# Kernel tuning notes

Measured on AMD Instinct MI355X. Metric: run time of the kernel, lower is better.

## Reference

```python
import jax, jax.numpy as jnp
import numpy as np
from math import log

MODEL_DIM = 512
NUM_HEADS = 8
DIM_HEAD = 64
INNER = NUM_HEADS * DIM_HEAD
B, L = 8, 1024
EPS = 1e-5


def setup_inputs() -> dict:
    key = jax.random.key(0)
    ks = jax.random.split(key, 9)
    x = jax.random.normal(ks[0], (B, L, MODEL_DIM), dtype=jnp.float32)
    gamma = jnp.ones((MODEL_DIM,), jnp.float32)
    beta = jnp.zeros((MODEL_DIM,), jnp.float32)
    w_qkv = jax.random.normal(ks[1], (3 * INNER, MODEL_DIM), jnp.float32) * (MODEL_DIM ** -0.5)
    b_qkv = jnp.zeros((3 * INNER,), jnp.float32)
    w_pos = jax.random.normal(ks[2], (INNER, MODEL_DIM), jnp.float32) * (MODEL_DIM ** -0.5)
    w_out = jax.random.normal(ks[3], (MODEL_DIM, INNER), jnp.float32) * (INNER ** -0.5)
    b_out = jnp.zeros((MODEL_DIM,), jnp.float32)
    # xavier_uniform for (num_heads, dim_head)
    bound = (6.0 / (NUM_HEADS + DIM_HEAD)) ** 0.5
    u_bias = jax.random.uniform(ks[4], (NUM_HEADS, DIM_HEAD), jnp.float32, -bound, bound)
    v_bias = jax.random.uniform(ks[5], (NUM_HEADS, DIM_HEAD), jnp.float32, -bound, bound)
    return {"x": x, "gamma": gamma, "beta": beta, "w_qkv": w_qkv, "b_qkv": b_qkv,
            "w_pos": w_pos, "w_out": w_out, "b_out": b_out, "u_bias": u_bias, "v_bias": v_bias}


def _rel_pos_emb(seq_len, d):
    # (L, D): (i - j) scaled by sinusoid frequencies, then cos on even cols, sin on odd cols
    rel = (jnp.arange(seq_len, dtype=jnp.float32)[:, None]
           - jnp.arange(d, dtype=jnp.float32)[None, :])
    freqs = jnp.exp(-jnp.arange(0, 2 * d, 2, dtype=jnp.float32) * (log(10000.0) / MODEL_DIM))
    angle = rel * freqs[None, :]
    even = (jnp.arange(d) % 2) == 0
    return jnp.where(even[None, :], jnp.cos(angle), jnp.sin(angle))  # (L, D)


def reference(x, gamma, beta, w_qkv, b_qkv, w_pos, w_out, b_out, u_bias, v_bias):
    b, l, d = x.shape
    h, dh = NUM_HEADS, DIM_HEAD
    # LayerNorm
    mu = jnp.mean(x, axis=-1, keepdims=True)
    var = jnp.mean(jnp.square(x - mu), axis=-1, keepdims=True)
    xn = (x - mu) * jax.lax.rsqrt(var + EPS) * gamma + beta
    # relative position embedding, identical per batch element
    pe = _rel_pos_emb(l, d)                      # (L, D)
    pos = (pe @ w_pos.T).reshape(l, h, dh)       # (L, H, Dh)
    pos = jnp.transpose(pos, (1, 0, 2))          # (H, L, Dh)
    # qkv
    qkv = xn @ w_qkv.T + b_qkv                   # (B, L, 3*inner)
    q, k, v = jnp.split(qkv, 3, axis=-1)
    def to_heads(t):
        return jnp.transpose(t.reshape(b, l, h, dh), (0, 2, 1, 3))  # (B,H,L,Dh)
    q, k, v = to_heads(q), to_heads(k), to_heads(v)
    scale = dh ** -0.5
    content = jnp.einsum('bhld,bhmd->bhlm', q + u_bias[None, :, None, :], k)
    pos_score = jnp.einsum('bhld,hmd->bhlm', q + v_bias[None, :, None, :], pos)
    attn = jax.nn.softmax((content + pos_score) * scale, axis=-1)
    out = jnp.einsum('bhlm,bhmd->bhld', attn, v)
    out = jnp.transpose(out, (0, 2, 1, 3)).reshape(b, l, h * dh)
    return out @ w_out.T + b_out  # dropout p=0.0 -> identity
```

## Files before the change

### kernel.cpp

```cpp
#include <hip/hip_runtime.h>
#include <math.h>

static constexpr int Bn = 8, Ln = 1024, Dm = 512, Hn = 8, DhN = 64;

typedef short bf16x8 __attribute__((ext_vector_type(8)));
typedef float f32x4 __attribute__((ext_vector_type(4)));
typedef _Float16 f16x4 __attribute__((ext_vector_type(4)));
typedef _Float16 f16x8 __attribute__((ext_vector_type(8)));
typedef unsigned int u32x4 __attribute__((ext_vector_type(4)));
typedef unsigned short u16x8 __attribute__((ext_vector_type(8)));

#define QSCALE 0.1803368801111137f

static __device__ __forceinline__ unsigned short f2b(float f) {
  union { float f; unsigned int u; } x;
  x.f = f;
  unsigned int u = x.u;
  unsigned int r = (u + 0x7FFFu + ((u >> 16) & 1u)) >> 16;
  return (unsigned short)r;
}
static __device__ __forceinline__ float b2f(unsigned short u) {
  union { unsigned int u; float f; } x;
  x.u = ((unsigned int)u) << 16;
  return x.f;
}

#define GLDS16(g, l)                                                        \
  __builtin_amdgcn_global_load_lds((const __attribute__((address_space(1))) void*)(g), \
                                   (__attribute__((address_space(3))) void*)(l), 16, 0, 0)

__global__ __launch_bounds__(256) void prep1(const float* __restrict__ x,
                                             const float* __restrict__ gamma,
                                             const float* __restrict__ beta,
                                             unsigned short* __restrict__ xn,
                                             unsigned short* __restrict__ pe,
                                             const float* __restrict__ wq, unsigned short* __restrict__ wqb,
                                             const float* __restrict__ wp, unsigned short* __restrict__ wpb,
                                             const float* __restrict__ wo, unsigned short* __restrict__ wob) {
  int b = blockIdx.x;
  int t = threadIdx.x;
  if (b < 8192) {
    const float2 v = *(const float2*)(x + (size_t)b * Dm + t * 2);
    float s = v.x + v.y;
    float sq = v.x * v.x + v.y * v.y;
#pragma unroll
    for (int off = 32; off > 0; off >>= 1) {
      s += __shfl_down(s, off);
      sq += __shfl_down(sq, off);
    }
    __shared__ float red[8];
    int wave = t >> 6, lane = t & 63;
    if (lane == 0) { red[wave * 2] = s; red[wave * 2 + 1] = sq; }
    __syncthreads();
    float S = red[0] + red[2] + red[4] + red[6];
    float SQ = red[1] + red[3] + red[5] + red[7];
    float mu = S * (1.0f / Dm);
    float var = SQ * (1.0f / Dm) - mu * mu;
    float rstd = rsqrtf(var + 1e-5f);
    int c = t * 2;
    ushort2 o;
    o.x = f2b((v.x - mu) * rstd * gamma[c] + beta[c]);
    o.y = f2b((v.y - mu) * rstd * gamma[c + 1] + beta[c + 1]);
    *(ushort2*)(xn + (size_t)b * Dm + c) = o;
  } else if (b < 10240) {
    int idx = (b - 8192) * 256 + t;
    int l = idx >> 9, k = idx & 511;
    float freq = __expf(-0.0359778921f * (float)k);
    float angle = (float)(l - k) * freq;
    pe[idx] = f2b((k & 1) ? __sinf(angle) : __cosf(angle));
  } else {
    int cb = b - 10240;
    const float* src;
    unsigned short* dst;
    int off;
    if (cb < 768) { src = wq; dst = wqb; off = cb; }
    else if (cb < 1024) { src = wp; dst = wpb; off = cb - 768; }
    else { src = wo; dst = wob; off = cb - 1024; }
    int i = off * 256 + t;
    float4 v = *(const float4*)(src + (size_t)i * 4);
    ushort4 o;
    o.x = f2b(v.x); o.y = f2b(v.y); o.z = f2b(v.z); o.w = f2b(v.w);
    *(ushort4*)(dst + (size_t)i * 4) = o;
  }
}

__global__ __launch_bounds__(256, 6) void gemm2(const unsigned short* __restrict__ Ain,
                                                const unsigned short* __restrict__ Bwin,
                                                const float* __restrict__ biasin,
                                                unsigned short* __restrict__ oq,
                                                unsigned short* __restrict__ ok,
                                                unsigned short* __restrict__ ov,
                                                const unsigned short* __restrict__ A2,
                                                const unsigned short* __restrict__ B2,
                                                unsigned short* __restrict__ outp) {
  int by = blockIdx.y, bx = blockIdx.x;
  int mode = 0;
  const unsigned short* A = Ain;
  const unsigned short* Bw = Bwin;
  const float* bias = biasin;
  if (by < 64) {
    int lid = by * 24 + bx;
    int i = lid >> 3;
    by = (lid & 7) * 8 + i / 24;
    bx = i % 24;
  } else {
    if (bx >= 8) return;
    A = A2; Bw = B2; bias = nullptr; mode = 1; by -= 64;
  }
  const int K = 512;
  __shared__ alignas(16) unsigned short As[128 * 64];
  __shared__ alignas(16) unsigned short Bs[64 * 64];
  const int t = threadIdx.x;
  const int lane = t & 63, w = t >> 6;
  const int c = lane & 15, q8 = lane >> 4;
  const int wm = (w & 1) * 64, wn = (w >> 1) * 32;
  const int m0 = by * 128, n0 = bx * 64;

  f32x4 acc[4][2];
#pragma unroll
  for (int i = 0; i < 4; ++i)
#pragma unroll
    for (int j = 0; j < 2; ++j) acc[i][j] = (f32x4){0.f, 0.f, 0.f, 0.f};

  const int srow = lane >> 3;
  const int sgr = (lane & 7) ^ srow;

  for (int k0 = 0; k0 < K; k0 += 64) {
    __syncthreads();
#pragma unroll
    for (int s = 0; s < 4; ++s) {
      int r = s * 32 + w * 8 + srow;
      GLDS16(A + (size_t)(m0 + r) * K + k0 + sgr * 8, As + (s * 256 + w * 64 + lane) * 8);
    }
#pragma unroll
    for (int s = 0; s < 2; ++s) {
      int r = s * 32 + w * 8 + srow;
      GLDS16(Bw + (size_t)(n0 + r) * K + k0 + sgr * 8, Bs + (s * 256 + w * 64 + lane) * 8);
    }
    __syncthreads();
#pragma unroll
    for (int kk = 0; kk < 2; ++kk) {
      bf16x8 a[4], b[2];
      const int q = kk * 4 + q8;
#pragma unroll
      for (int i = 0; i < 4; ++i) {
        int r = wm + i * 16 + c;
        a[i] = *(const bf16x8*)&As[(r * 8 + (q ^ (r & 7))) * 8];
      }
#pragma unroll
      for (int j = 0; j < 2; ++j) {
        int r = wn + j * 16 + c;
        b[j] = *(const bf16x8*)&Bs[(r * 8 + (q ^ (r & 7))) * 8];
      }
#pragma unroll
      for (int i = 0; i < 4; ++i)
#pragma unroll
        for (int j = 0; j < 2; ++j)
          acc[i][j] = __builtin_amdgcn_mfma_f32_16x16x32_bf16(a[i], b[j], acc[i][j], 0, 0, 0);
    }
  }
#pragma unroll
  for (int i = 0; i < 4; ++i) {
#pragma unroll
    for (int r = 0; r < 4; ++r) {
      int m = m0 + wm + i * 16 + q8 * 4 + r;
#pragma unroll
      for (int j = 0; j < 2; ++j) {
        int n = n0 + wn + j * 16 + c;
        float val = acc[i][j][r] + (bias ? bias[n] : 0.0f);
        if (mode == 0) {
          int part = n >> 9, h = (n >> 6) & 7, dh = n & 63;
          int bb = m >> 10, l = m & 1023;
          size_t idx = (size_t)((bb * 8 + h) * 1024 + l) * 64 + dh;
          if (part == 0) {
            oq[idx] = f2b(val * QSCALE);
          } else if (part == 1) {
            ok[idx] = f2b(val);
          } else {
            union { _Float16 h; unsigned short u; } cv;
            cv.h = (_Float16)val;
            ov[idx] = cv.u;
          }
        } else {
          int h = n >> 6, dh = n & 63;
          outp[(size_t)(h * 1024 + m) * 64 + dh] = f2b(val);
        }
      }
    }
  }
}

__global__ __launch_bounds__(256, 8) void gemm_mfma(const unsigned short* __restrict__ Ain,
                                                    const unsigned short* __restrict__ Bwin,
                                                    const float* __restrict__ biasin,
                                                    float* __restrict__ outfin,
                                                    int K) {
  int by = blockIdx.y, bx = blockIdx.x;
  {
    int NBX = gridDim.x;
    int lid = by * NBX + bx;
    int i = lid >> 3;
    by = (lid & 7) * 16 + i / NBX;
    bx = i % NBX;
  }
  const unsigned short* A = Ain;
  const unsigned short* Bw = Bwin;
  const float* bias = biasin;
  float* outf = outfin;
  __shared__ alignas(16) unsigned short As[64 * 64];
  __shared__ alignas(16) unsigned short Bs[64 * 64];
  const int t = threadIdx.x;
  const int lane = t & 63, w = t >> 6;
  const int c = lane & 15, q8 = lane >> 4;
  const int wm = (w & 1) * 32, wn = (w >> 1) * 32;
  const int m0 = by * 64, n0 = bx * 64;

  f32x4 acc[2][2];
#pragma unroll
  for (int i = 0; i < 2; ++i)
#pragma unroll
    for (int j = 0; j < 2; ++j) acc[i][j] = (f32x4){0.f, 0.f, 0.f, 0.f};

  const int srow = lane >> 3;
  const int sgr = (lane & 7) ^ srow;

  for (int k0 = 0; k0 < K; k0 += 64) {
    __syncthreads();
#pragma unroll
    for (int j = 0; j < 2; ++j) {
      int r = j * 32 + w * 8 + srow;
      GLDS16(A + (size_t)(m0 + r) * K + k0 + sgr * 8, As + (j * 256 + w * 64 + lane) * 8);
      GLDS16(Bw + (size_t)(n0 + r) * K + k0 + sgr * 8, Bs + (j * 256 + w * 64 + lane) * 8);
    }
    __syncthreads();
#pragma unroll
    for (int kk = 0; kk < 2; ++kk) {
      bf16x8 a[2], b[2];
      const int q = kk * 4 + q8;
#pragma unroll
      for (int i = 0; i < 2; ++i) {
        int r = wm + i * 16 + c;
        a[i] = *(const bf16x8*)&As[(r * 8 + (q ^ (r & 7))) * 8];
      }
#pragma unroll
      for (int j = 0; j < 2; ++j) {
        int r = wn + j * 16 + c;
        b[j] = *(const bf16x8*)&Bs[(r * 8 + (q ^ (r & 7))) * 8];
      }
#pragma unroll
      for (int i = 0; i < 2; ++i)
#pragma unroll
        for (int j = 0; j < 2; ++j)
          acc[i][j] = __builtin_amdgcn_mfma_f32_16x16x32_bf16(a[i], b[j], acc[i][j], 0, 0, 0);
    }
  }
#pragma unroll
  for (int i = 0; i < 2; ++i) {
#pragma unroll
    for (int r = 0; r < 4; ++r) {
      int m = m0 + wm + i * 16 + q8 * 4 + r;
#pragma unroll
      for (int j = 0; j < 2; ++j) {
        int n = n0 + wn + j * 16 + c;
        outf[(size_t)m * 512 + n] = acc[i][j][r] + bias[n];
      }
    }
  }
}

__global__ __launch_bounds__(256) void prep2(unsigned short* __restrict__ kbuf,
                                             const unsigned short* __restrict__ posbf,
                                             const float* __restrict__ ub,
                                             const float* __restrict__ vbb,
                                             float* __restrict__ biasout,
                                             const unsigned short* __restrict__ v,
                                             unsigned short* __restrict__ vt) {
  int b = blockIdx.x;
  int t = threadIdx.x;
  if (b < 2048) {
    int g = b * 32 + (t >> 3);
    int s = t & 7;
    int h = (g >> 10) & 7;
    int m = g & 1023;
    u16x8 kv8 = *(const u16x8*)(kbuf + (size_t)g * 64 + s * 8);
    u16x8 pv8 = *(const u16x8*)(posbf + (size_t)(h * 1024 + m) * 64 + s * 8);
    f32x4 u0 = *(const f32x4*)(ub + h * 64 + s * 8);
    f32x4 u1 = *(const f32x4*)(ub + h * 64 + s * 8 + 4);
    f32x4 v0 = *(const f32x4*)(vbb + h * 64 + s * 8);
    f32x4 v1 = *(const f32x4*)(vbb + h * 64 + s * 8 + 4);
    float part = 0.0f;
    u16x8 o8;
#pragma unroll
    for (int e = 0; e < 8; ++e) {
      float kf = b2f(kv8[e]);
      float pf = b2f(pv8[e]);
      float ue = (e < 4) ? u0[e] : u1[e - 4];
      float ve = (e < 4) ? v0[e] : v1[e - 4];
      part += ue * kf + ve * pf;
      o8[e] = f2b(kf + pf);
    }
    *(u16x8*)(kbuf + (size_t)g * 64 + s * 8) = o8;
    part += __shfl_xor(part, 1);
    part += __shfl_xor(part, 2);
    part += __shfl_xor(part, 4);
    if (s == 0) biasout[g] = part * QSCALE;
  } else {
    __shared__ unsigned short Ts[64 * 68];
    int bb = b - 2048;
    int bh = bb >> 4, lt = bb & 15;
    const unsigned short* vg = v + (size_t)bh * 65536 + lt * 4096;
#pragma unroll
    for (int s = 0; s < 4; ++s) {
      int idx = t + s * 256;
      int r = idx >> 4, c4 = (idx & 15) << 2;
      *(ushort4*)&Ts[r * 68 + c4] = *(const ushort4*)(vg + r * 64 + c4);
    }
    __syncthreads();
#pragma unroll
    for (int s = 0; s < 4; ++s) {
      int idx = t + s * 256;
      int d = idx >> 4, l4 = (idx & 15) << 2;
      ushort4 o;
      o.x = Ts[(l4 + 0) * 68 + d];
      o.y = Ts[(l4 + 1) * 68 + d];
      o.z = Ts[(l4 + 2) * 68 + d];
      o.w = Ts[(l4 + 3) * 68 + d];
      int pb = ((l4 >> 5) & 1) * 32 + ((l4 >> 2) & 3) * 8 + ((l4 >> 4) & 1) * 4;
      *(ushort4*)(vt + (size_t)bh * 65536 + d * 1024 + lt * 64 + pb) = o;
    }
  }
}

__global__ __launch_bounds__(256, 2) void flash_mfma(const unsigned short* __restrict__ qbf,
                                                     const unsigned short* __restrict__ kbf,
                                                     const unsigned short* __restrict__ vt,
                                                     const float* __restrict__ bias,
                                                     unsigned short* __restrict__ attn_out) {
  __shared__ alignas(16) unsigned short Ks[2][64 * 64];
  __shared__ alignas(16) unsigned short Vs[2][64 * 64];
  __shared__ alignas(16) float Bls[1024];
  const int t = threadIdx.x;
  const int lane = t & 63, w = t >> 6;
  const int c = lane & 15, q8 = lane >> 4;
  const int cc7 = c & 7;
  const int lid = blockIdx.x + (blockIdx.y << 3);
  const int bh = ((lid & 7) << 3) + ((lid >> 3) & 7);
  const int qt = lid >> 6;
  const unsigned short* qg = qbf + (size_t)bh * 65536;
  const unsigned short* kg = kbf + (size_t)bh * 65536;
  const unsigned short* vg = vt + (size_t)bh * 65536;
  const float* bg = bias + (size_t)bh * 1024;

  GLDS16(bg + t * 4, Bls + t * 4);

  bf16x8 bq[2][2];
#pragma unroll
  for (int g = 0; g < 2; ++g) {
    int qlg = qt * 128 + g * 64 + w * 16 + c;
    bq[g][0] = *(const bf16x8*)(qg + (size_t)qlg * 64 + q8 * 8);
    bq[g][1] = *(const bf16x8*)(qg + (size_t)qlg * 64 + 32 + q8 * 8);
  }

  float m_st[2] = {-INFINITY, -INFINITY};
  float l_st[2] = {0.0f, 0.0f};
  f32x4 o[2][4];
#pragma unroll
  for (int g = 0; g < 2; ++g)
#pragma unroll
    for (int i = 0; i < 4; ++i) o[g][i] = (f32x4){0.f, 0.f, 0.f, 0.f};

  const int srow = lane >> 3;
  const int sgr = (lane & 7) ^ srow;
  const int r0 = w * 16 + srow;

  u32x4 pk[2][2], pv[2][2];
#pragma unroll
  for (int h = 0; h < 2; ++h)
#pragma unroll
    for (int j = 0; j < 2; ++j) {
      int r = r0 + j * 8;
      pk[h][j] = *(const u32x4*)(kg + (size_t)(h * 64 + r) * 64 + sgr * 8);
      pv[h][j] = *(const u32x4*)(vg + (size_t)r * 1024 + h * 64 + sgr * 8);
    }

  for (int it = 0; it < 8; ++it) {
    __syncthreads();
#pragma unroll
    for (int h = 0; h < 2; ++h)
#pragma unroll
      for (int j = 0; j < 2; ++j) {
        int r = r0 + j * 8;
        *(u32x4*)&Ks[h][(r * 8 + (lane & 7)) * 8] = pk[h][j];
        *(u32x4*)&Vs[h][(r * 8 + (lane & 7)) * 8] = pv[h][j];
      }
    __syncthreads();
    if (it < 7) {
#pragma unroll
      for (int h = 0; h < 2; ++h)
#pragma unroll
        for (int j = 0; j < 2; ++j) {
          int r = r0 + j * 8;
          pk[h][j] = *(const u32x4*)(kg + (size_t)((it + 1) * 128 + h * 64 + r) * 64 + sgr * 8);
          pv[h][j] = *(const u32x4*)(vg + (size_t)r * 1024 + (it + 1) * 128 + h * 64 + sgr * 8);
        }
    }

    f32x4 sc[2][2][4];
#pragma unroll
    for (int h = 0; h < 2; ++h) {
#pragma unroll
      for (int nt = 0; nt < 4; ++nt) {
        f32x4 ci = *(const f32x4*)&Bls[it * 128 + h * 64 + nt * 16 + q8 * 4];
        const int row = nt * 16 + c;
        bf16x8 ak0 = *(const bf16x8*)&Ks[h][(row * 8 + (q8 ^ cc7)) * 8];
        bf16x8 ak1 = *(const bf16x8*)&Ks[h][(row * 8 + ((q8 + 4) ^ cc7)) * 8];
#pragma unroll
        for (int g = 0; g < 2; ++g) {
          f32x4 z = __builtin_amdgcn_mfma_f32_16x16x32_bf16(ak0, bq[g][0], ci, 0, 0, 0);
          sc[g][h][nt] = __builtin_amdgcn_mfma_f32_16x16x32_bf16(ak1, bq[g][1], z, 0, 0, 0);
        }
      }
    }
    float mx[2];
#pragma unroll
    for (int g = 0; g < 2; ++g) {
      float m = sc[g][0][0][0];
#pragma unroll
      for (int h = 0; h < 2; ++h)
#pragma unroll
        for (int nt = 0; nt < 4; ++nt)
#pragma unroll
          for (int r = 0; r < 4; ++r) m = fmaxf(m, sc[g][h][nt][r]);
      mx[g] = m;
    }
    {
      float s0 = __shfl_xor(mx[0], 16);
      float s1 = __shfl_xor(mx[1], 16);
      mx[0] = fmaxf(mx[0], s0);
      mx[1] = fmaxf(mx[1], s1);
      s0 = __shfl_xor(mx[0], 32);
      s1 = __shfl_xor(mx[1], 32);
      mx[0] = fmaxf(mx[0], s0);
      mx[1] = fmaxf(mx[1], s1);
    }
    f16x8 pf8[2][2][2];
#pragma unroll
    for (int g = 0; g < 2; ++g) {
      float mn = fmaxf(m_st[g], mx[g]);
      float al = __builtin_amdgcn_exp2f(m_st[g] - mn);
      float su = 0.0f;
#pragma unroll
      for (int h = 0; h < 2; ++h)
#pragma unroll
        for (int nt = 0; nt < 4; ++nt)
#pragma unroll
          for (int r = 0; r < 4; ++r) {
            float p = __builtin_amdgcn_exp2f(sc[g][h][nt][r] - mn);
            su += p;
            pf8[g][h][nt >> 1][((nt & 1) << 2) | r] = (_Float16)p;
          }
      l_st[g] = l_st[g] * al + su;
      m_st[g] = mn;
#pragma unroll
      for (int i = 0; i < 4; ++i) o[g][i] *= al;
    }
#pragma unroll
    for (int i = 0; i < 4; ++i) {
      const int row = i * 16 + c;
#pragma unroll
      for (int h = 0; h < 2; ++h) {
        f16x8 va = *(const f16x8*)&Vs[h][(row * 8 + (q8 ^ cc7)) * 8];
        f16x8 vb = *(const f16x8*)&Vs[h][(row * 8 + ((4 + q8) ^ cc7)) * 8];
#pragma unroll
        for (int g = 0; g < 2; ++g) {
          o[g][i] = __builtin_amdgcn_mfma_f32_16x16x32_f16(va, pf8[g][h][0], o[g][i], 0, 0, 0);
          o[g][i] = __builtin_amdgcn_mfma_f32_16x16x32_f16(vb, pf8[g][h][1], o[g][i], 0, 0, 0);
        }
      }
    }
  }
  float lt0 = l_st[0], lt1 = l_st[1];
  {
    float s0 = __shfl_xor(lt0, 16);
    float s1 = __shfl_xor(lt1, 16);
    lt0 += s0; lt1 += s1;
    s0 = __shfl_xor(lt0, 32);
    s1 = __shfl_xor(lt1, 32);
    lt0 += s0; lt1 += s1;
  }
  const int bidx = bh >> 3, h = bh & 7;
#pragma unroll
  for (int g = 0; g < 2; ++g) {
    int qlg = qt * 128 + g * 64 + w * 16 + c;
    float inv = 1.0f / (g == 0 ? lt0 : lt1);
    size_t base = (size_t)(bidx * 1024 + qlg) * 512 + h * 64;
#pragma unroll
    for (int i = 0; i < 4; ++i) {
      ushort4 ov4;
      ov4.x = f2b(o[g][i][0] * inv);
      ov4.y = f2b(o[g][i][1] * inv);
      ov4.z = f2b(o[g][i][2] * inv);
      ov4.w = f2b(o[g][i][3] * inv);
      *(ushort4*)(attn_out + base + i * 16 + q8 * 4) = ov4;
    }
  }
}

extern "C" void kernel_launch(void* const* d_in, const int* in_sizes, int n_in,
                              void* d_out, int out_size, void* d_ws, size_t ws_size,
                              hipStream_t stream) {
  const float* x      = (const float*)d_in[0];
  const float* gamma  = (const float*)d_in[1];
  const float* beta   = (const float*)d_in[2];
  const float* w_qkv  = (const float*)d_in[3];
  const float* b_qkv  = (const float*)d_in[4];
  const float* w_pos  = (const float*)d_in[5];
  const float* w_out  = (const float*)d_in[6];
  const float* b_out  = (const float*)d_in[7];
  const float* u_bias = (const float*)d_in[8];
  const float* v_bias = (const float*)d_in[9];
  float* out = (float*)d_out;

  unsigned short* wsu = (unsigned short*)d_ws;
  unsigned short* xnb   = wsu;
  unsigned short* peb   = wsu + 4194304;
  unsigned short* wqkvb = wsu + 4718592;
  unsigned short* wposb = wsu + 5505024;
  unsigned short* woutb = wsu + 5767168;
  unsigned short* qbf   = wsu + 6291456;
  unsigned short* kbf   = wsu + 10485760;
  unsigned short* vbf   = wsu + 14680064;
  unsigned short* vtb   = wsu + 18874368;
  unsigned short* attnb = wsu + 23068672;
  unsigned short* posbf = wsu + 27262976;
  float* biasb = (float*)(wsu + 28311552);

  prep1<<<11520, 256, 0, stream>>>(x, gamma, beta, xnb, peb,
                                   w_qkv, wqkvb, w_pos, wposb, w_out, woutb);
  gemm2<<<dim3(24, 72), 256, 0, stream>>>(xnb, wqkvb, b_qkv, qbf, kbf, vbf,
                                          peb, wposb, posbf);
  prep2<<<3072, 256, 0, stream>>>(kbf, posbf, u_bias, v_bias, biasb, vbf, vtb);
  flash_mfma<<<dim3(8, 64), 256, 0, stream>>>(qbf, kbf, vtb, biasb, attnb);
  gemm_mfma<<<dim3(8, 128), 256, 0, stream>>>(attnb, woutb, b_out, out, 512);
}
```

Before: 162.1 us.

## Retile QKV GEMM to 64x64 with K=128 steps; vectorize LayerNorm to two rows per block

The QKV/pos GEMM moves from 128x64 tiles with a 64-deep K step to 64x64 tiles with a 128-deep K step. This doubles the grid and halves the per-wave accumulator count, with a 16-way LDS swizzle to match and the occupancy hint lowered to 5. LayerNorm now processes two rows per block using float4 loads and vectorized gamma/beta reads, which halves the block count for that section. The smaller tiles mean less operand reuse per block, traded for more parallelism and fewer K-loop barriers.

```diff
diff --git a/kernel.cpp b/kernel.cpp
--- a/kernel.cpp
+++ b/kernel.cpp
@@ -39,10 +39,12 @@
                                              const float* __restrict__ wo, unsigned short* __restrict__ wob) {
   int b = blockIdx.x;
   int t = threadIdx.x;
-  if (b < 8192) {
-    const float2 v = *(const float2*)(x + (size_t)b * Dm + t * 2);
-    float s = v.x + v.y;
-    float sq = v.x * v.x + v.y * v.y;
+  if (b < 4096) {
+    int row = b * 2 + (t >> 7);
+    int tl = t & 127;
+    const float4 v = *(const float4*)(x + (size_t)row * Dm + tl * 4);
+    float s = v.x + v.y + v.z + v.w;
+    float sq = v.x * v.x + v.y * v.y + v.z * v.z + v.w * v.w;
 #pragma unroll
     for (int off = 32; off > 0; off >>= 1) {
       s += __shfl_down(s, off);
@@ -52,24 +54,29 @@
     int wave = t >> 6, lane = t & 63;
     if (lane == 0) { red[wave * 2] = s; red[wave * 2 + 1] = sq; }
     __syncthreads();
-    float S = red[0] + red[2] + red[4] + red[6];
-    float SQ = red[1] + red[3] + red[5] + red[7];
+    int half = t >> 7;
+    float S = red[half * 4 + 0] + red[half * 4 + 2];
+    float SQ = red[half * 4 + 1] + red[half * 4 + 3];
     float mu = S * (1.0f / Dm);
     float var = SQ * (1.0f / Dm) - mu * mu;
     float rstd = rsqrtf(var + 1e-5f);
-    int c = t * 2;
-    ushort2 o;
-    o.x = f2b((v.x - mu) * rstd * gamma[c] + beta[c]);
-    o.y = f2b((v.y - mu) * rstd * gamma[c + 1] + beta[c + 1]);
-    *(ushort2*)(xn + (size_t)b * Dm + c) = o;
-  } else if (b < 10240) {
-    int idx = (b - 8192) * 256 + t;
+    int c = tl * 4;
+    const float4 g4 = *(const float4*)(gamma + c);
+    const float4 b4 = *(const float4*)(beta + c);
+    ushort4 o;
+    o.x = f2b((v.x - mu) * rstd * g4.x + b4.x);
+    o.y = f2b((v.y - mu) * rstd * g4.y + b4.y);
+    o.z = f2b((v.z - mu) * rstd * g4.z + b4.z);
+    o.w = f2b((v.w - mu) * rstd * g4.w + b4.w);
+    *(ushort4*)(xn + (size_t)row * Dm + c) = o;
+  } else if (b < 6144) {
+    int idx = (b - 4096) * 256 + t;
     int l = idx >> 9, k = idx & 511;
     float freq = __expf(-0.0359778921f * (float)k);
     float angle = (float)(l - k) * freq;
     pe[idx] = f2b((k & 1) ? __sinf(angle) : __cosf(angle));
   } else {
-    int cb = b - 10240;
+    int cb = b - 6144;
     const float* src;
     unsigned short* dst;
     int off;
@@ -84,7 +91,7 @@
   }
 }
 
-__global__ __launch_bounds__(256, 6) void gemm2(const unsigned short* __restrict__ Ain,
+__global__ __launch_bounds__(256, 5) void gemm2(const unsigned short* __restrict__ Ain,
                                                 const unsigned short* __restrict__ Bwin,
                                                 const float* __restrict__ biasin,
                                                 unsigned short* __restrict__ oq,
@@ -98,69 +105,65 @@
   const unsigned short* A = Ain;
   const unsigned short* Bw = Bwin;
   const float* bias = biasin;
-  if (by < 64) {
+  if (by < 128) {
     int lid = by * 24 + bx;
     int i = lid >> 3;
-    by = (lid & 7) * 8 + i / 24;
+    by = (lid & 7) * 16 + i / 24;
     bx = i % 24;
   } else {
     if (bx >= 8) return;
-    A = A2; Bw = B2; bias = nullptr; mode = 1; by -= 64;
+    A = A2; Bw = B2; bias = nullptr; mode = 1; by -= 128;
   }
   const int K = 512;
-  __shared__ alignas(16) unsigned short As[128 * 64];
-  __shared__ alignas(16) unsigned short Bs[64 * 64];
+  __shared__ alignas(16) unsigned short As[64 * 128];
+  __shared__ alignas(16) unsigned short Bs[64 * 128];
   const int t = threadIdx.x;
   const int lane = t & 63, w = t >> 6;
   const int c = lane & 15, q8 = lane >> 4;
-  const int wm = (w & 1) * 64, wn = (w >> 1) * 32;
-  const int m0 = by * 128, n0 = bx * 64;
-
-  f32x4 acc[4][2];
-#pragma unroll
-  for (int i = 0; i < 4; ++i)
+  const int wm = (w & 1) * 32, wn = (w >> 1) * 32;
+  const int m0 = by * 64, n0 = bx * 64;
+
+  f32x4 acc[2][2];
+#pragma unroll
+  for (int i = 0; i < 2; ++i)
 #pragma unroll
     for (int j = 0; j < 2; ++j) acc[i][j] = (f32x4){0.f, 0.f, 0.f, 0.f};
 
-  const int srow = lane >> 3;
-  const int sgr = (lane & 7) ^ srow;
-
-  for (int k0 = 0; k0 < K; k0 += 64) {
-    __syncthreads();
-#pragma unroll
-    for (int s = 0; s < 4; ++s) {
-      int r = s * 32 + w * 8 + srow;
-      GLDS16(A + (size_t)(m0 + r) * K + k0 + sgr * 8, As + (s * 256 + w * 64 + lane) * 8);
-    }
-#pragma unroll
-    for (int s = 0; s < 2; ++s) {
-      int r = s * 32 + w * 8 + srow;
-      GLDS16(Bw + (size_t)(n0 + r) * K + k0 + sgr * 8, Bs + (s * 256 + w * 64 + lane) * 8);
-    }
-    __syncthreads();
-#pragma unroll
-    for (int kk = 0; kk < 2; ++kk) {
-      bf16x8 a[4], b[2];
+  const int srow = t >> 4;
+  const int sgr = (t & 15) ^ srow;
+
+  for (int k0 = 0; k0 < K; k0 += 128) {
+    __syncthreads();
+#pragma unroll
+    for (int p = 0; p < 4; ++p) {
+      int r = p * 16 + srow;
+      GLDS16(A + (size_t)(m0 + r) * K + k0 + sgr * 8, As + (p * 256 + t) * 8);
+      GLDS16(Bw + (size_t)(n0 + r) * K + k0 + sgr * 8, Bs + (p * 256 + t) * 8);
+    }
+    __syncthreads();
+#pragma unroll
+    for (int kk = 0; kk < 4; ++kk) {
+      bf16x8 a[2], b[2];
       const int q = kk * 4 + q8;
 #pragma unroll
-      for (int i = 0; i < 4; ++i) {
+      for (int i = 0; i < 2; ++i) {
         int r = wm + i * 16 + c;
-        a[i] = *(const bf16x8*)&As[(r * 8 + (q ^ (r & 7))) * 8];
+        a[i] = *(const bf16x8*)&As[(r * 16 + (q ^ (r & 15))) * 8];
       }
 #pragma unroll
       for (int j = 0; j < 2; ++j) {
         int r = wn + j * 16 + c;
-        b[j] = *(const bf16x8*)&Bs[(r * 8 + (q ^ (r & 7))) * 8];
-      }
-#pragma unroll
-      for (int i = 0; i < 4; ++i)
+        b[j] = *(const bf16x8*)&Bs[(r * 16 + (q ^ (r & 15))) * 8];
+      }
+#pragma unroll
+      for (int i = 0; i < 2; ++i)
 #pragma unroll
         for (int j = 0; j < 2; ++j)
           acc[i][j] = __builtin_amdgcn_mfma_f32_16x16x32_bf16(a[i], b[j], acc[i][j], 0, 0, 0);
     }
   }
 #pragma unroll
-  for (int i = 0; i < 4; ++i) {
+  for (int i = 0; i < 2; ++i) {
 #pragma unroll
     for (int r = 0; r < 4; ++r) {
       int m = m0 + wm + i * 16 + q8 * 4 + r;
@@ -535,10 +538,10 @@
   unsigned short* posbf = wsu + 27262976;
   float* biasb = (float*)(wsu + 28311552);
 
-  prep1<<<11520, 256, 0, stream>>>(x, gamma, beta, xnb, peb,
-                                   w_qkv, wqkvb, w_pos, wposb, w_out, woutb);
-  gemm2<<<dim3(24, 72), 256, 0, stream>>>(xnb, wqkvb, b_qkv, qbf, kbf, vbf,
-                                          peb, wposb, posbf);
+  prep1<<<7424, 256, 0, stream>>>(x, gamma, beta, xnb, peb,
+                                  w_qkv, wqkvb, w_pos, wposb, w_out, woutb);
+  gemm2<<<dim3(24, 144), 256, 0, stream>>>(xnb, wqkvb, b_qkv, qbf, kbf, vbf,
+                                           peb, wposb, posbf);
   prep2<<<3072, 256, 0, stream>>>(kbf, posbf, u_bias, v_bias, biasb, vbf, vtb);
   flash_mfma<<<dim3(8, 64), 256, 0, stream>>>(qbf, kbf, vtb, biasb, attnb);
   gemm_mfma<<<dim3(8, 128), 256, 0, stream>>>(attnb, woutb, b_out, out, 512);
```

Result: no change. 163.3 us (+0.7%).
